# Optimization experiments

Hardware: AMD Instinct MI355X
Metric: run time of the kernel (lower is better)

## Reference

```python
import jax, jax.numpy as jnp
import numpy as np

B, SQ, SK = 2, 2048, 2048
D_MODEL, N_HEADS = 1024, 16
D_HEAD = D_MODEL // N_HEADS
LN_EPS = 1e-5


def _ln(x, w, b):
    # per-head LayerNorm over last dim (d_head)
    mu = jnp.mean(x, axis=-1, keepdims=True)
    var = jnp.mean(jnp.square(x - mu), axis=-1, keepdims=True)
    return (x - mu) * jax.lax.rsqrt(var + LN_EPS) * w + b


def setup_inputs() -> dict:
    key = jax.random.key(0)
    ks = jax.random.split(key, 8)
    sd = 1.0 / np.sqrt(D_MODEL)
    so = 1.0 / np.sqrt(D_HEAD)
    return {
        "x_q": jax.random.normal(ks[0], (B, SQ, D_MODEL), jnp.float32),
        "x_kv": jax.random.normal(ks[1], (B, SK, D_MODEL), jnp.float32),
        "mask": jnp.tril(jnp.ones((SQ, SK), dtype=bool)),  # causal
        "W_Q": jax.random.normal(ks[2], (N_HEADS, D_MODEL, D_HEAD), jnp.float32) * sd,
        "W_K": jax.random.normal(ks[3], (N_HEADS, D_MODEL, D_HEAD), jnp.float32) * sd,
        "W_V": jax.random.normal(ks[4], (N_HEADS, D_MODEL, D_HEAD), jnp.float32) * sd,
        "W_O": jax.random.normal(ks[5], (N_HEADS, D_HEAD, D_MODEL), jnp.float32) * so,
        "b_Q": jnp.zeros((N_HEADS, D_HEAD), jnp.float32),
        "b_K": jnp.zeros((N_HEADS, D_HEAD), jnp.float32),
        "b_V": jnp.zeros((N_HEADS, D_HEAD), jnp.float32),
        "b_O": jnp.zeros((D_MODEL,), jnp.float32),
        "ln1_w": jnp.ones((D_HEAD,), jnp.float32),
        "ln1_b": jnp.zeros((D_HEAD,), jnp.float32),
        "ln2_w": jnp.ones((D_HEAD,), jnp.float32),
        "ln2_b": jnp.zeros((D_HEAD,), jnp.float32),
    }


def reference(x_q, x_kv, mask, W_Q, W_K, W_V, W_O, b_Q, b_K, b_V, b_O,
              ln1_w, ln1_b, ln2_w, ln2_b):
    # QKV projections: b s d, n d h -> b s n h
    q = jnp.einsum('bsd,ndh->bsnh', x_q, W_Q) + b_Q
    k = jnp.einsum('bsd,ndh->bsnh', x_kv, W_K) + b_K
    v = jnp.einsum('bsd,ndh->bsnh', x_kv, W_V) + b_V
    # QK-norm (ln_first=False, rope=None -> just apply LN after projections)
    q = _ln(q, ln1_w, ln1_b)
    k = _ln(k, ln2_w, ln2_b)
    # NOTE: no 1/sqrt(d_head) scaling, matching the original module
    att = jnp.einsum('bqnh,bknh->bnqk', q, k)
    att = jnp.where(mask, att, -jnp.inf)
    probas = jax.nn.softmax(att, axis=-1)
    z = jnp.einsum('bnqk,bknh->bqnh', probas, v)
    out = jnp.einsum('bqnh,nhd->bqd', z, W_O) + b_O
    return (out, k, v)
```

## Files before the change

kernel.cpp:

```cpp
#include <hip/hip_runtime.h>
#include <hip/hip_bf16.h>

#define B_   2
#define SQ_  2048
#define DM_  1024
#define NH_  16
#define DH_  64

typedef __attribute__((ext_vector_type(8))) short          bf16x8;
typedef __attribute__((ext_vector_type(8))) unsigned short u16x8;
typedef __attribute__((ext_vector_type(4))) float          f32x4;

__device__ __forceinline__ unsigned short f2bf(float f) {
    union { __hip_bfloat16 h; unsigned short u; } c;
    c.h = __float2bfloat16(f);
    return c.u;
}
__device__ __forceinline__ float gsum16(float v) {
    v += __shfl_xor(v, 1);
    v += __shfl_xor(v, 2);
    v += __shfl_xor(v, 4);
    v += __shfl_xor(v, 8);
    return v;
}

__device__ __forceinline__ void gll16(const unsigned short* g, unsigned short* l) {
    __builtin_amdgcn_global_load_lds(
        (const __attribute__((address_space(1))) unsigned int*)g,
        (__attribute__((address_space(3))) unsigned int*)l,
        16, 0, 0);
}

__global__ __launch_bounds__(256) void prep_all(
    const float* __restrict__ W_Q, const float* __restrict__ W_K,
    const float* __restrict__ W_V, const float* __restrict__ W_O,
    const float* __restrict__ x_q, const float* __restrict__ x_kv,
    unsigned short* __restrict__ WTq, unsigned short* __restrict__ WTkv,
    unsigned short* __restrict__ WTo,
    unsigned short* __restrict__ xqbf, unsigned short* __restrict__ xkvbf)
{
    const int bid = blockIdx.x, tid = threadIdx.x;
    if (bid >= 1024) {
        const int cid = bid - 1024;
        const float* src = (cid < 256) ? x_q : x_kv;
        unsigned short* dst = (cid < 256) ? xqbf : xkvbf;
        const size_t base = (size_t)(cid & 255) * 16384 + tid * 4;
#pragma unroll
        for (int i = 0; i < 16; ++i) {
            const float4 v = *(const float4*)(src + base + i * 1024);
            ushort4 o;
            o.x = f2bf(v.x); o.y = f2bf(v.y); o.z = f2bf(v.z); o.w = f2bf(v.w);
            *(ushort4*)(dst + base + i * 1024) = o;
        }
        return;
    }
    __shared__ float t[64][65];
    const float* src; unsigned short* dst; int R, C, r0, c0;
    if (bid < 768) {
        const int which = bid >> 8, rem = bid & 255;
        const int rblk = rem & 15, zz = rem >> 4;
        src = (which == 0) ? W_Q : (which == 1) ? W_K : W_V;
        dst = (which == 0) ? WTq : (which == 1) ? WTkv : (WTkv + (1u << 20));
        src += (size_t)65536 * zz;
        dst += (size_t)65536 * zz;
        R = 1024; C = 64; r0 = rblk * 64; c0 = 0;
    } else {
        const int rem = bid - 768;
        src = W_O; dst = WTo; R = 1024; C = 1024;
        r0 = (rem & 15) * 64; c0 = (rem >> 4) * 64;
    }
    const int lr = tid >> 6, lc = tid & 63;
#pragma unroll
    for (int i = 0; i < 16; ++i)
        t[lr + i * 4][lc] = src[(size_t)(r0 + lr + i * 4) * C + c0 + lc];
    __syncthreads();
#pragma unroll
    for (int i = 0; i < 16; ++i)
        dst[(size_t)(c0 + lr + i * 4) * R + r0 + lc] = f2bf(t[lc][lr + i * 4]);
}

template <int TN, int MODE>
__device__ __forceinline__ void gemm_body(
    unsigned short (*__restrict__ As)[64], unsigned short (*__restrict__ Bs)[64],
    int bx, int by, const unsigned short* __restrict__ Abf,
    const unsigned short* __restrict__ WT,
    const float* __restrict__ biasK, const float* __restrict__ biasV,
    const float* __restrict__ lnw, const float* __restrict__ lnb,
    float* __restrict__ Cf, float* __restrict__ Cf2,
    unsigned short* __restrict__ Cb, unsigned short* __restrict__ CbT, int tid)
{
    constexpr int MI = (TN == 128) ? 4 : 2;
    constexpr int BP = TN / 64;

    const int m0 = by * 128;
    const int c0 = bx * TN;

    const int wid = tid >> 6, lane = tid & 63;
    const int wm = (TN == 128) ? (wid >> 1) * 64 : wid * 32;
    const int wn = (TN == 128) ? (wid & 1) * 64 : 0;
    const int l15 = lane & 15, qd = lane >> 4;

    const int srow  = tid >> 3;
    const int pslot = tid & 7;
    const int sslot = pslot ^ (srow & 7);
    const unsigned short* Ag = Abf + (size_t)(m0 + srow) * 1024 + sslot * 8;
    const unsigned short* Bg = WT  + (size_t)(c0 + srow) * 1024 + sslot * 8;
    unsigned short* Al = &As[srow][pslot * 8];
    unsigned short* Bl = &Bs[srow][pslot * 8];

    const f32x4 zero4 = {0.f, 0.f, 0.f, 0.f};
    f32x4 acc[MI][4];
#pragma unroll
    for (int mi = 0; mi < MI; ++mi)
#pragma unroll
        for (int ni = 0; ni < 4; ++ni) acc[mi][ni] = zero4;

    const int r7 = l15 & 7;

    for (int kb = 0; kb < 16; ++kb) {
        const size_t kof = (size_t)kb * 64;
        __syncthreads();
#pragma unroll
        for (int j = 0; j < 4; ++j)
            gll16(Ag + (size_t)j * 32 * 1024 + kof, Al + j * 32 * 64);
#pragma unroll
        for (int j = 0; j < 2 * BP; ++j)
            gll16(Bg + (size_t)j * 32 * 1024 + kof, Bl + j * 32 * 64);
        __syncthreads();
#pragma unroll
        for (int ks = 0; ks < 2; ++ks) {
            const int cs = ((ks * 4 + qd) ^ r7) * 8;
            bf16x8 af[MI], bfr[4];
#pragma unroll
            for (int mi = 0; mi < MI; ++mi)
                af[mi] = *(const bf16x8*)&As[wm + mi * 16 + l15][cs];
#pragma unroll
            for (int ni = 0; ni < 4; ++ni)
                bfr[ni] = *(const bf16x8*)&Bs[wn + ni * 16 + l15][cs];
#pragma unroll
            for (int mi = 0; mi < MI; ++mi)
#pragma unroll
                for (int ni = 0; ni < 4; ++ni)
                    acc[mi][ni] = __builtin_amdgcn_mfma_f32_16x16x32_bf16(
                        af[mi], bfr[ni], acc[mi][ni], 0, 0, 0);
        }
    }

    const float* bias = (MODE == 1 && c0 >= 1024) ? biasV : biasK;
    float bv[4];
#pragma unroll
    for (int ni = 0; ni < 4; ++ni) bv[ni] = bias[(c0 + wn + ni * 16 + l15) & 1023];
#pragma unroll
    for (int mi = 0; mi < MI; ++mi)
#pragma unroll
        for (int ni = 0; ni < 4; ++ni)
#pragma unroll
            for (int r = 0; r < 4; ++r) acc[mi][ni][r] += bv[ni];

    if constexpr (MODE != 2) {
        const bool doLN = (MODE == 0) || (c0 < 1024);
        if (doLN) {
            float w4[4], lb4[4];
#pragma unroll
            for (int ni = 0; ni < 4; ++ni) {
                w4[ni]  = lnw[ni * 16 + l15];
                lb4[ni] = lnb[ni * 16 + l15];
            }
#pragma unroll
            for (int mi = 0; mi < MI; ++mi)
#pragma unroll
                for (int r = 0; r < 4; ++r) {
                    float s1 = acc[mi][0][r] + acc[mi][1][r] + acc[mi][2][r] + acc[mi][3][r];
                    const float mu = gsum16(s1) * (1.0f / 64.0f);
                    float s2 = acc[mi][0][r] * acc[mi][0][r] + acc[mi][1][r] * acc[mi][1][r]
                             + acc[mi][2][r] * acc[mi][2][r] + acc[mi][3][r] * acc[mi][3][r];
                    const float var = gsum16(s2) * (1.0f / 64.0f) - mu * mu;
                    const float rstd = rsqrtf(var + 1e-5f);
#pragma unroll
                    for (int ni = 0; ni < 4; ++ni)
                        acc[mi][ni][r] = (acc[mi][ni][r] - mu) * rstd * w4[ni] + lb4[ni];
                }
        }
    }

    if constexpr (MODE == 0) {
#pragma unroll
        for (int mi = 0; mi < MI; ++mi)
#pragma unroll
            for (int r = 0; r < 4; ++r) {
                const size_t grow = m0 + wm + mi * 16 + qd * 4 + r;
#pragma unroll
                for (int ni = 0; ni < 4; ++ni)
                    Cb[grow * 1024 + c0 + wn + ni * 16 + l15] = f2bf(acc[mi][ni][r]);
            }
    } else if constexpr (MODE == 2) {
#pragma unroll
        for (int mi = 0; mi < MI; ++mi)
#pragma unroll
            for (int r = 0; r < 4; ++r) {
                const size_t grow = m0 + wm + mi * 16 + qd * 4 + r;
#pragma unroll
                for (int ni = 0; ni < 4; ++ni)
                    Cf[grow * 1024 + c0 + wn + ni * 16 + l15] = acc[mi][ni][r];
            }
    } else {
        if (c0 < 1024) {
#pragma unroll
            for (int mi = 0; mi < MI; ++mi)
#pragma unroll
                for (int r = 0; r < 4; ++r) {
                    const size_t grow = m0 + wm + mi * 16 + qd * 4 + r;
#pragma unroll
                    for (int ni = 0; ni < 4; ++ni) {
                        const int gcol = c0 + wn + ni * 16 + l15;
                        Cf[grow * 1024 + gcol] = acc[mi][ni][r];
                        Cb[grow * 1024 + gcol] = f2bf(acc[mi][ni][r]);
                    }
                }
        } else {
#pragma unroll
            for (int mi = 0; mi < MI; ++mi) {
                const int growb = m0 + wm + mi * 16 + qd * 4;
                const int bb_ = growb >> 11, ss = growb & 2047;
#pragma unroll
                for (int ni = 0; ni < 4; ++ni) {
                    const int gv = c0 - 1024 + wn + ni * 16 + l15;
                    const int hh = gv >> 6, dd = gv & 63;
#pragma unroll
                    for (int r = 0; r < 4; ++r)
                        Cf2[(size_t)(growb + r) * 1024 + gv] = acc[mi][ni][r];
                    ushort4 w;
                    w.x = f2bf(acc[mi][ni][0]); w.y = f2bf(acc[mi][ni][1]);
                    w.z = f2bf(acc[mi][ni][2]); w.w = f2bf(acc[mi][ni][3]);
                    *(ushort4*)&CbT[(((size_t)bb_ * NH_ + hh) * DH_ + dd) * SQ_ + ss] = w;
                }
            }
        }
    }
}

__global__ __launch_bounds__(256) void qkv_fused(
    const unsigned short* __restrict__ xqbf, const unsigned short* __restrict__ xkvbf,
    const unsigned short* __restrict__ WTq, const unsigned short* __restrict__ WTkv,
    const float* __restrict__ b_Q, const float* __restrict__ b_K,
    const float* __restrict__ b_V,
    const float* __restrict__ ln1w, const float* __restrict__ ln1b,
    const float* __restrict__ ln2w, const float* __restrict__ ln2b,
    float* __restrict__ kout, float* __restrict__ vout,
    unsigned short* __restrict__ qz, unsigned short* __restrict__ kbf,
    unsigned short* __restrict__ vbfT)
{
    __shared__ __align__(16) unsigned short As[128][64];
    __shared__ __align__(16) unsigned short Bs[128][64];
    const int bid = blockIdx.x, tid = threadIdx.x;
    if (bid < 512) {
        gemm_body<128, 1>(As, Bs, bid & 15, bid >> 4, xkvbf, WTkv, b_K, b_V,
                          ln2w, ln2b, kout, vout, kbf, vbfT, tid);
    } else {
        const int b2 = bid - 512;
        gemm_body<128, 0>(As, Bs, b2 & 7, b2 >> 3, xqbf, WTq, b_Q, nullptr,
                          ln1w, ln1b, nullptr, nullptr, qz, nullptr, tid);
    }
}

__global__ __launch_bounds__(256) void o_gemm(
    const unsigned short* __restrict__ zbf, const unsigned short* __restrict__ WTo,
    const float* __restrict__ b_O, float* __restrict__ out)
{
    __shared__ __align__(16) unsigned short As[128][64];
    __shared__ __align__(16) unsigned short Bs[64][64];
    gemm_body<64, 2>(As, Bs, blockIdx.x, blockIdx.y, zbf, WTo, b_O, nullptr,
                     nullptr, nullptr, out, nullptr, nullptr, nullptr, threadIdx.x);
}

__global__ __launch_bounds__(256) void attn_mfma(
    unsigned short* __restrict__ qz, const unsigned short* __restrict__ kbf,
    const unsigned short* __restrict__ vbfT)
{
    __shared__ __align__(16) unsigned short Ks[2][64][72];
    __shared__ __align__(16) unsigned short VsT[2][64][72];
    __shared__ __align__(16) unsigned short Ps[64][72];

    const int tid = threadIdx.x;
    const int h = blockIdx.y, b = blockIdx.z;
    const int wid = tid >> 6, lane = tid & 63;
    const int l15 = lane & 15, qd = lane >> 4;
    const int srow = tid >> 2, scol = (tid & 3) * 16;

    const size_t kbase = (size_t)b * SQ_ * DM_ + (size_t)h * DH_;
    const size_t vbase = ((size_t)b * NH_ + h) * DH_ * (size_t)SQ_;
    const f32x4 zero4 = {0.f, 0.f, 0.f, 0.f};

    for (int pass = 0; pass < 2; ++pass) {
        const int qt = pass ? blockIdx.x : 31 - blockIdx.x;

        bf16x8 qf[2];
        {
            const unsigned short* qp =
                qz + kbase + (size_t)(qt * 64 + wid * 16 + l15) * DM_ + qd * 8;
            qf[0] = *(const bf16x8*)(qp);
            qf[1] = *(const bf16x8*)(qp + 32);
        }

        f32x4 z[4];
#pragma unroll
        for (int ni = 0; ni < 4; ++ni) z[ni] = zero4;
        float m_i = -3.0e38f, l_i = 0.f;

        {
            const unsigned short* ks = kbf + kbase + (size_t)srow * DM_ + scol;
            const u16x8 a0 = *(const u16x8*)(ks);
            const u16x8 a1 = *(const u16x8*)(ks + 8);
            const unsigned short* vs = vbfT + vbase + (size_t)srow * SQ_ + scol;
            const u16x8 b0 = *(const u16x8*)(vs);
            const u16x8 b1 = *(const u16x8*)(vs + 8);
            *(u16x8*)&Ks[0][srow][scol + 0]  = a0;
            *(u16x8*)&Ks[0][srow][scol + 8]  = a1;
            *(u16x8*)&VsT[0][srow][scol + 0] = b0;
            *(u16x8*)&VsT[0][srow][scol + 8] = b1;
        }
        __syncthreads();

        for (int kt = 0; kt <= qt; ++kt) {
            const int cur = kt & 1;

            u16x8 kr0, kr1, vr0, vr1;
            if (kt < qt) {
                const unsigned short* ks =
                    kbf + kbase + (size_t)((kt + 1) * 64 + srow) * DM_ + scol;
                kr0 = *(const u16x8*)(ks);
                kr1 = *(const u16x8*)(ks + 8);
                const unsigned short* vs =
                    vbfT + vbase + (size_t)srow * SQ_ + (kt + 1) * 64 + scol;
                vr0 = *(const u16x8*)(vs);
                vr1 = *(const u16x8*)(vs + 8);
            }

            f32x4 s[4];
#pragma unroll
            for (int mi = 0; mi < 4; ++mi) s[mi] = zero4;
#pragma unroll
            for (int ks2 = 0; ks2 < 2; ++ks2)
#pragma unroll
                for (int mi = 0; mi < 4; ++mi) {
                    const bf16x8 af =
                        *(const bf16x8*)&Ks[cur][mi * 16 + l15][ks2 * 32 + qd * 8];
                    s[mi] = __builtin_amdgcn_mfma_f32_16x16x32_bf16(af, qf[ks2], s[mi], 0, 0, 0);
                }

            if (kt == qt) {
#pragma unroll
                for (int mi = 0; mi < 4; ++mi)
#pragma unroll
                    for (int r = 0; r < 4; ++r)
                        if (mi * 16 + qd * 4 + r > wid * 16 + l15) s[mi][r] = -3.0e38f;
            }

            float mloc = -3.0e38f;
#pragma unroll
            for (int mi = 0; mi < 4; ++mi)
#pragma unroll
                for (int r = 0; r < 4; ++r) mloc = fmaxf(mloc, s[mi][r]);
            mloc = fmaxf(mloc, __shfl_xor(mloc, 16));
            mloc = fmaxf(mloc, __shfl_xor(mloc, 32));
            const float mn = fmaxf(m_i, mloc);
            const float alpha = __expf(m_i - mn);
            float rs = 0.f;
#pragma unroll
            for (int mi = 0; mi < 4; ++mi)
#pragma unroll
                for (int r = 0; r < 4; ++r) {
                    const float e = __expf(s[mi][r] - mn);
                    s[mi][r] = e;
                    rs += e;
                }
            rs += __shfl_xor(rs, 16);
            rs += __shfl_xor(rs, 32);
            l_i = l_i * alpha + rs;
            m_i = mn;

#pragma unroll
            for (int mi = 0; mi < 4; ++mi) {
                ushort4 w;
                w.x = f2bf(s[mi][0]); w.y = f2bf(s[mi][1]);
                w.z = f2bf(s[mi][2]); w.w = f2bf(s[mi][3]);
                *(ushort4*)&Ps[wid * 16 + l15][mi * 16 + qd * 4] = w;
            }

#pragma unroll
            for (int r = 0; r < 4; ++r) {
                const float ar = __shfl(alpha, qd * 4 + r);
#pragma unroll
                for (int ni = 0; ni < 4; ++ni) z[ni][r] *= ar;
            }

#pragma unroll
            for (int ks2 = 0; ks2 < 2; ++ks2) {
                const bf16x8 ap = *(const bf16x8*)&Ps[wid * 16 + l15][ks2 * 32 + qd * 8];
#pragma unroll
                for (int ni = 0; ni < 4; ++ni) {
                    const bf16x8 bv =
                        *(const bf16x8*)&VsT[cur][ni * 16 + l15][ks2 * 32 + qd * 8];
                    z[ni] = __builtin_amdgcn_mfma_f32_16x16x32_bf16(ap, bv, z[ni], 0, 0, 0);
                }
            }

            if (kt < qt) {
                *(u16x8*)&Ks[cur ^ 1][srow][scol + 0]  = kr0;
                *(u16x8*)&Ks[cur ^ 1][srow][scol + 8]  = kr1;
                *(u16x8*)&VsT[cur ^ 1][srow][scol + 0] = vr0;
                *(u16x8*)&VsT[cur ^ 1][srow][scol + 8] = vr1;
            }
            __syncthreads();
        }

        const float linv = 1.0f / l_i;
#pragma unroll
        for (int r = 0; r < 4; ++r) {
            const float lr_ = __shfl(linv, qd * 4 + r);
            const size_t row = (size_t)qt * 64 + wid * 16 + qd * 4 + r;
#pragma unroll
            for (int ni = 0; ni < 4; ++ni)
                qz[kbase + row * DM_ + ni * 16 + l15] = f2bf(z[ni][r] * lr_);
        }
    }
}

extern "C" void kernel_launch(void* const* d_in, const int* in_sizes, int n_in,
                              void* d_out, int out_size, void* d_ws, size_t ws_size,
                              hipStream_t stream)
{
    const float* x_q  = (const float*)d_in[0];
    const float* x_kv = (const float*)d_in[1];
    const float* W_Q  = (const float*)d_in[3];
    const float* W_K  = (const float*)d_in[4];
    const float* W_V  = (const float*)d_in[5];
    const float* W_O  = (const float*)d_in[6];
    const float* b_Q  = (const float*)d_in[7];
    const float* b_K  = (const float*)d_in[8];
    const float* b_V  = (const float*)d_in[9];
    const float* b_O  = (const float*)d_in[10];
    const float* ln1w = (const float*)d_in[11];
    const float* ln1b = (const float*)d_in[12];
    const float* ln2w = (const float*)d_in[13];
    const float* ln2b = (const float*)d_in[14];

    const size_t NTOK = (size_t)B_ * SQ_;
    float* out  = (float*)d_out;
    float* kout = out + NTOK * DM_;
    float* vout = kout + NTOK * DM_;

    unsigned short* xqbf  = (unsigned short*)out;
    unsigned short* xkvbf = xqbf + (1u << 22);

    unsigned short* wsu  = (unsigned short*)d_ws;
    unsigned short* WTq  = wsu;
    unsigned short* WTkv = WTq + (1u << 20);
    unsigned short* WTo  = WTkv + (2u << 20);
    unsigned short* qz   = WTo + (1u << 20);
    unsigned short* kbf  = qz + (1u << 22);
    unsigned short* vbfT = kbf + (1u << 22);

    prep_all<<<1536, 256, 0, stream>>>(W_Q, W_K, W_V, W_O, x_q, x_kv,
                                       WTq, WTkv, WTo, xqbf, xkvbf);

    qkv_fused<<<768, 256, 0, stream>>>(xqbf, xkvbf, WTq, WTkv, b_Q, b_K, b_V,
                                       ln1w, ln1b, ln2w, ln2b,
                                       kout, vout, qz, kbf, vbfT);

    attn_mfma<<<dim3(16, NH_, B_), 256, 0, stream>>>(qz, kbf, vbfT);

    o_gemm<<<dim3(16, 32), 256, 0, stream>>>(qz, WTo, b_O, out);
}
```

Measured before the change: 246.1 us.

## Double-buffer GEMM LDS tiles and unify O-projection to 128x128 tiles

```diff
diff --git a/kernel.cpp b/kernel.cpp
--- a/kernel.cpp
+++ b/kernel.cpp
@@ -79,9 +79,10 @@
         dst[(size_t)(c0 + lr + i * 4) * R + r0 + lc] = f2bf(t[lc][lr + i * 4]);
 }
 
-template <int TN, int MODE>
+template <int MODE>
 __device__ __forceinline__ void gemm_body(
-    unsigned short (*__restrict__ As)[64], unsigned short (*__restrict__ Bs)[64],
+    unsigned short* __restrict__ As,
+    unsigned short* __restrict__ Bs,
     int bx, int by, const unsigned short* __restrict__ Abf,
     const unsigned short* __restrict__ WT,
     const float* __restrict__ biasK, const float* __restrict__ biasV,
@@ -89,15 +90,12 @@
     float* __restrict__ Cf, float* __restrict__ Cf2,
     unsigned short* __restrict__ Cb, unsigned short* __restrict__ CbT, int tid)
 {
-    constexpr int MI = (TN == 128) ? 4 : 2;
-    constexpr int BP = TN / 64;
-
     const int m0 = by * 128;
-    const int c0 = bx * TN;
+    const int c0 = bx * 128;
 
     const int wid = tid >> 6, lane = tid & 63;
-    const int wm = (TN == 128) ? (wid >> 1) * 64 : wid * 32;
-    const int wn = (TN == 128) ? (wid & 1) * 64 : 0;
+    const int wm = (wid >> 1) * 64;
+    const int wn = (wid & 1) * 64;
     const int l15 = lane & 15, qd = lane >> 4;
 
     const int srow  = tid >> 3;
@@ -105,53 +103,71 @@
     const int sslot = pslot ^ (srow & 7);
     const unsigned short* Ag = Abf + (size_t)(m0 + srow) * 1024 + sslot * 8;
     const unsigned short* Bg = WT  + (size_t)(c0 + srow) * 1024 + sslot * 8;
-    unsigned short* Al = &As[srow][pslot * 8];
-    unsigned short* Bl = &Bs[srow][pslot * 8];
+    unsigned short* Al = As + srow * 64 + pslot * 8;
+    unsigned short* Bl = Bs + srow * 64 + pslot * 8;
 
     const f32x4 zero4 = {0.f, 0.f, 0.f, 0.f};
-    f32x4 acc[MI][4];
-#pragma unroll
-    for (int mi = 0; mi < MI; ++mi)
+    f32x4 acc[4][4];
+#pragma unroll
+    for (int mi = 0; mi < 4; ++mi)
 #pragma unroll
         for (int ni = 0; ni < 4; ++ni) acc[mi][ni] = zero4;
 
     const int r7 = l15 & 7;
 
+#define STAGE(kb, bi)                                                          \
+    {                                                                          \
+        const size_t kof = (size_t)(kb) * 64;                                  \
+        const int bo = (bi) * 8192;                                            \
+        _Pragma("unroll")                                                      \
+        for (int j = 0; j < 4; ++j)                                            \
+            gll16(Ag + (size_t)j * 32 * 1024 + kof, Al + bo + j * 32 * 64);    \
+        _Pragma("unroll")                                                      \
+        for (int j = 0; j < 4; ++j)                                            \
+            gll16(Bg + (size_t)j * 32 * 1024 + kof, Bl + bo + j * 32 * 64);    \
+    }
+#define PIPE_BAR()                                                             \
+    {                                                                          \
+        asm volatile("s_waitcnt vmcnt(0)" ::: "memory");                       \
+        __builtin_amdgcn_sched_barrier(0);                                     \
+        __builtin_amdgcn_s_barrier();                                          \
+        __builtin_amdgcn_sched_barrier(0);                                     \
+    }
+
+    STAGE(0, 0)
+    PIPE_BAR()
+
     for (int kb = 0; kb < 16; ++kb) {
-        const size_t kof = (size_t)kb * 64;
-        __syncthreads();
-#pragma unroll
-        for (int j = 0; j < 4; ++j)
-            gll16(Ag + (size_t)j * 32 * 1024 + kof, Al + j * 32 * 64);
-#pragma unroll
-        for (int j = 0; j < 2 * BP; ++j)
-            gll16(Bg + (size_t)j * 32 * 1024 + kof, Bl + j * 32 * 64);
-        __syncthreads();
+        const int cur = kb & 1;
+        if (kb < 15) STAGE(kb + 1, cur ^ 1)
 #pragma unroll
         for (int ks = 0; ks < 2; ++ks) {
             const int cs = ((ks * 4 + qd) ^ r7) * 8;
-            bf16x8 af[MI], bfr[4];
-#pragma unroll
-            for (int mi = 0; mi < MI; ++mi)
-                af[mi] = *(const bf16x8*)&As[wm + mi * 16 + l15][cs];
+            bf16x8 af[4], bfr[4];
+#pragma unroll
+            for (int mi = 0; mi < 4; ++mi)
+                af[mi] = *(const bf16x8*)(As + cur * 8192 + (wm + mi * 16 + l15) * 64 + cs);
 #pragma unroll
             for (int ni = 0; ni < 4; ++ni)
-                bfr[ni] = *(const bf16x8*)&Bs[wn + ni * 16 + l15][cs];
-#pragma unroll
-            for (int mi = 0; mi < MI; ++mi)
+                bfr[ni] = *(const bf16x8*)(Bs + cur * 8192 + (wn + ni * 16 + l15) * 64 + cs);
+#pragma unroll
+            for (int mi = 0; mi < 4; ++mi)
 #pragma unroll
                 for (int ni = 0; ni < 4; ++ni)
                     acc[mi][ni] = __builtin_amdgcn_mfma_f32_16x16x32_bf16(
                         af[mi], bfr[ni], acc[mi][ni], 0, 0, 0);
         }
-    }
+        PIPE_BAR()
+    }
+#undef STAGE
+#undef PIPE_BAR
 
     const float* bias = (MODE == 1 && c0 >= 1024) ? biasV : biasK;
     float bv[4];
 #pragma unroll
     for (int ni = 0; ni < 4; ++ni) bv[ni] = bias[(c0 + wn + ni * 16 + l15) & 1023];
 #pragma unroll
-    for (int mi = 0; mi < MI; ++mi)
+    for (int mi = 0; mi < 4; ++mi)
 #pragma unroll
         for (int ni = 0; ni < 4; ++ni)
 #pragma unroll
@@ -167,7 +183,7 @@
                 lb4[ni] = lnb[ni * 16 + l15];
             }
 #pragma unroll
-            for (int mi = 0; mi < MI; ++mi)
+            for (int mi = 0; mi < 4; ++mi)
 #pragma unroll
                 for (int r = 0; r < 4; ++r) {
                     float s1 = acc[mi][0][r] + acc[mi][1][r] + acc[mi][2][r] + acc[mi][3][r];
@@ -185,7 +201,7 @@
 
     if constexpr (MODE == 0) {
 #pragma unroll
-        for (int mi = 0; mi < MI; ++mi)
+        for (int mi = 0; mi < 4; ++mi)
 #pragma unroll
             for (int r = 0; r < 4; ++r) {
                 const size_t grow = m0 + wm + mi * 16 + qd * 4 + r;
@@ -195,7 +211,7 @@
             }
     } else if constexpr (MODE == 2) {
 #pragma unroll
-        for (int mi = 0; mi < MI; ++mi)
+        for (int mi = 0; mi < 4; ++mi)
 #pragma unroll
             for (int r = 0; r < 4; ++r) {
                 const size_t grow = m0 + wm + mi * 16 + qd * 4 + r;
@@ -206,7 +222,7 @@
     } else {
         if (c0 < 1024) {
 #pragma unroll
-            for (int mi = 0; mi < MI; ++mi)
+            for (int mi = 0; mi < 4; ++mi)
 #pragma unroll
                 for (int r = 0; r < 4; ++r) {
                     const size_t grow = m0 + wm + mi * 16 + qd * 4 + r;
@@ -219,7 +235,7 @@
                 }
         } else {
 #pragma unroll
-            for (int mi = 0; mi < MI; ++mi) {
+            for (int mi = 0; mi < 4; ++mi) {
                 const int growb = m0 + wm + mi * 16 + qd * 4;
                 const int bb_ = growb >> 11, ss = growb & 2047;
 #pragma unroll
@@ -250,16 +266,16 @@
     unsigned short* __restrict__ qz, unsigned short* __restrict__ kbf,
     unsigned short* __restrict__ vbfT)
 {
-    __shared__ __align__(16) unsigned short As[128][64];
-    __shared__ __align__(16) unsigned short Bs[128][64];
+    __shared__ __align__(16) unsigned short As[2 * 128 * 64];
+    __shared__ __align__(16) unsigned short Bs[2 * 128 * 64];
     const int bid = blockIdx.x, tid = threadIdx.x;
     if (bid < 512) {
-        gemm_body<128, 1>(As, Bs, bid & 15, bid >> 4, xkvbf, WTkv, b_K, b_V,
-                          ln2w, ln2b, kout, vout, kbf, vbfT, tid);
+        gemm_body<1>(As, Bs, bid & 15, bid >> 4, xkvbf, WTkv, b_K, b_V,
+                     ln2w, ln2b, kout, vout, kbf, vbfT, tid);
     } else {
         const int b2 = bid - 512;
-        gemm_body<128, 0>(As, Bs, b2 & 7, b2 >> 3, xqbf, WTq, b_Q, nullptr,
-                          ln1w, ln1b, nullptr, nullptr, qz, nullptr, tid);
+        gemm_body<0>(As, Bs, b2 & 7, b2 >> 3, xqbf, WTq, b_Q, nullptr,
+                     ln1w, ln1b, nullptr, nullptr, qz, nullptr, tid);
     }
 }
 
@@ -267,10 +283,10 @@
     const unsigned short* __restrict__ zbf, const unsigned short* __restrict__ WTo,
     const float* __restrict__ b_O, float* __restrict__ out)
 {
-    __shared__ __align__(16) unsigned short As[128][64];
-    __shared__ __align__(16) unsigned short Bs[64][64];
-    gemm_body<64, 2>(As, Bs, blockIdx.x, blockIdx.y, zbf, WTo, b_O, nullptr,
-                     nullptr, nullptr, out, nullptr, nullptr, nullptr, threadIdx.x);
+    __shared__ __align__(16) unsigned short As[2 * 128 * 64];
+    __shared__ __align__(16) unsigned short Bs[2 * 128 * 64];
+    gemm_body<2>(As, Bs, blockIdx.x, blockIdx.y, zbf, WTo, b_O, nullptr,
+                 nullptr, nullptr, out, nullptr, nullptr, nullptr, threadIdx.x);
 }
 
 __global__ __launch_bounds__(256) void attn_mfma(
@@ -470,5 +486,5 @@
 
     attn_mfma<<<dim3(16, NH_, B_), 256, 0, stream>>>(qz, kbf, vbfT);
 
-    o_gemm<<<dim3(16, 32), 256, 0, stream>>>(qz, WTo, b_O, out);
-}
+    o_gemm<<<dim3(8, 32), 256, 0, stream>>>(qz, WTo, b_O, out);
+}
```

Result: slower. 267.8 us (+8.8%).
